# Kernel optimization log

Hardware: AMD Instinct MI355X
Metric: run time of the kernel (lower is better)

## Reference

```python
import jax, jax.numpy as jnp
import numpy as np

WIN = (8, 8)
NUM_HEADS = 8
DIM = 256


def _relative_position_index(wh, ww):
    ch = np.arange(wh)
    cw = np.arange(ww)
    coords = np.stack(np.meshgrid(ch, cw, indexing='ij'))  # [2, wh, ww]
    cf = coords.reshape(2, -1)                              # [2, N]
    rel = cf[:, :, None] - cf[:, None, :]                   # [2, N, N]
    rel = rel.transpose(1, 2, 0).copy()
    rel[:, :, 0] += wh - 1
    rel[:, :, 1] += ww - 1
    rel[:, :, 0] *= 2 * ww - 1
    return rel.sum(-1).astype(np.int32)                     # [N, N]


def setup_inputs() -> dict:
    key = jax.random.key(0)
    ks = jax.random.split(key, 7)
    N = WIN[0] * WIN[1]
    BW = 4096  # num_windows * batch
    x = jax.random.normal(ks[0], (BW, N, DIM), dtype=jnp.float32)
    # 0 / -inf style shift mask; random 0 or -100 per entry for generality
    mask = jnp.where(jax.random.uniform(ks[1], (BW, N, N)) < 0.2, -100.0, 0.0).astype(jnp.float32)
    rpb_table = jax.random.normal(ks[2], ((2 * WIN[0] - 1) * (2 * WIN[1] - 1), NUM_HEADS), dtype=jnp.float32) * 0.02
    qkv_w = jax.random.normal(ks[3], (3 * DIM, DIM), dtype=jnp.float32) * (DIM ** -0.5)
    qkv_b = jax.random.normal(ks[4], (3 * DIM,), dtype=jnp.float32) * 0.01
    proj_w = jax.random.normal(ks[5], (DIM, DIM), dtype=jnp.float32) * (DIM ** -0.5)
    proj_b = jax.random.normal(ks[6], (DIM,), dtype=jnp.float32) * 0.01
    rel_idx = jnp.asarray(_relative_position_index(*WIN))
    return {"x": x, "mask": mask, "rpb_table": rpb_table, "qkv_w": qkv_w,
            "qkv_b": qkv_b, "proj_w": proj_w, "proj_b": proj_b, "rel_idx": rel_idx}


def reference(x, mask, rpb_table, qkv_w, qkv_b, proj_w, proj_b, rel_idx):
    B_, N, C = x.shape
    H = NUM_HEADS
    hd = C // H
    scale = hd ** -0.5
    qkv = x @ qkv_w.T + qkv_b                               # [B_, N, 3C]
    qkv = qkv.reshape(B_, N, 3, H, hd).transpose(2, 0, 3, 1, 4)  # [3, B_, H, N, hd]
    q, k, v = qkv[0], qkv[1], qkv[2]
    attn = jnp.einsum('bhnd,bhmd->bhnm', q * scale, k)      # [B_, H, N, N]
    bias = rpb_table[rel_idx.reshape(-1)].reshape(N, N, H).transpose(2, 0, 1)  # [H, N, N]
    attn = attn + bias[None]
    nW = mask.shape[0]
    attn = attn.reshape(B_ // nW, nW, H, N, N) + mask[None, :, None]
    attn = attn.reshape(B_, H, N, N)
    attn = jax.nn.softmax(attn, axis=-1)
    out = jnp.einsum('bhnm,bhmd->bhnd', attn, v)            # [B_, H, N, hd]
    out = out.transpose(0, 2, 1, 3).reshape(B_, N, C)
    return out @ proj_w.T + proj_b
```

## Files before the change

### kernel.cpp

```cpp
#include <hip/hip_runtime.h>

typedef _Float16 half_t;
typedef __attribute__((ext_vector_type(8))) _Float16 half8;
typedef __attribute__((ext_vector_type(4))) float f32x4;

#define WS_W1   0
#define WS_W2   (768*256*2)
#define WS_BIAS (WS_W2 + 256*256*2)
#define QK_SCALE 0.17677669529663687f

__global__ __launch_bounds__(256) void prep_kernel(
    const float* __restrict__ qkv_w, const float* __restrict__ proj_w,
    const float* __restrict__ rpb, const int* __restrict__ rel_idx,
    char* __restrict__ ws) {
  int tid = blockIdx.x * 256 + threadIdx.x;
  half_t* W1 = (half_t*)(ws + WS_W1);
  half_t* W2 = (half_t*)(ws + WS_W2);
  float* BIASP = (float*)(ws + WS_BIAS);
  if (tid < 768 * 256) {
    int n = tid >> 8;
    float v = qkv_w[tid];
    if (n < 256) v *= QK_SCALE;
    W1[tid] = (half_t)v;
  }
  if (tid < 256 * 256) W2[tid] = (half_t)proj_w[tid];
  if (tid < 8 * 4096) {
    int r   = tid & 3;
    int l16 = (tid >> 2) & 15;
    int q   = (tid >> 6) & 3;
    int nt  = (tid >> 8) & 3;
    int mt  = (tid >> 10) & 3;
    int h   = (tid >> 12) & 7;
    int i = 16 * mt + 4 * q + r;
    int j = 16 * nt + l16;
    BIASP[tid] = rpb[rel_idx[i * 64 + j] * 8 + h];
  }
}

__global__ __launch_bounds__(512, 2) void fused_kernel(
    const float* __restrict__ x, const float* __restrict__ mask,
    const float* __restrict__ qkv_b, const float* __restrict__ proj_b,
    const char* __restrict__ ws, float* __restrict__ out, int nW) {
  __shared__ __align__(16) half_t Xs[64 * 264];
  __shared__ __align__(16) half_t QK[8][2][64 * 40];
  __shared__ __align__(16) half_t VT[8][32 * 72];
  __shared__ __align__(16) half_t Ms[64 * 68];

  const int b = blockIdx.x;
  const int tid = threadIdx.x;
  const int wave = tid >> 6, lane = tid & 63;
  const int l16 = lane & 15, quad = lane >> 4;
  const f32x4 z4 = {0.f, 0.f, 0.f, 0.f};

  {
    const float4* xw = (const float4*)(x + (size_t)b * 16384);
#pragma unroll
    for (int i = 0; i < 8; ++i) {
      int idx4 = tid + i * 512;
      float4 v = xw[idx4];
      int e = idx4 << 2;
      int row = e >> 8, col = e & 255;
      union { half_t h[4]; long long ll; } pk;
      pk.h[0] = (half_t)v.x; pk.h[1] = (half_t)v.y;
      pk.h[2] = (half_t)v.z; pk.h[3] = (half_t)v.w;
      *(long long*)(&Xs[row * 264 + col]) = pk.ll;
    }
    const float4* mw = (const float4*)(mask + (size_t)(b % nW) * 4096);
#pragma unroll
    for (int i = 0; i < 2; ++i) {
      int idx4 = tid + i * 512;
      float4 v = mw[idx4];
      int e = idx4 << 2;
      int mi = e >> 6, mj = e & 63;
      union { half_t h[4]; long long ll; } pk;
      pk.h[0] = (half_t)v.x; pk.h[1] = (half_t)v.y;
      pk.h[2] = (half_t)v.z; pk.h[3] = (half_t)v.w;
      *(long long*)(&Ms[mi * 68 + mj]) = pk.ll;
    }
  }
  __syncthreads();

  {
    const half_t* W1 = (const half_t*)(ws + WS_W1);
    const int nwb = wave * 96;
    f32x4 acc[6][4];
#pragma unroll
    for (int nt = 0; nt < 6; ++nt)
#pragma unroll
      for (int mt = 0; mt < 4; ++mt) acc[nt][mt] = z4;
#pragma unroll
    for (int ks = 0; ks < 8; ++ks) {
      half8 af[4];
#pragma unroll
      for (int mt = 0; mt < 4; ++mt)
        af[mt] = *(const half8*)(&Xs[(16 * mt + l16) * 264 + 32 * ks + quad * 8]);
#pragma unroll
      for (int nt = 0; nt < 6; ++nt) {
        half8 bf = *(const half8*)(&W1[(size_t)(nwb + 16 * nt + l16) * 256 + 32 * ks + quad * 8]);
#pragma unroll
        for (int mt = 0; mt < 4; ++mt)
          acc[nt][mt] = __builtin_amdgcn_mfma_f32_16x16x32_f16(af[mt], bf, acc[nt][mt], 0, 0, 0);
      }
    }
#pragma unroll
    for (int nt = 0; nt < 6; ++nt) {
      int n = nwb + 16 * nt + l16;
      float bias = qkv_b[n];
      int part = n >> 8;
      if (part == 0) bias *= QK_SCALE;
      int h = (n >> 5) & 7;
      int d = n & 31;
#pragma unroll
      for (int mt = 0; mt < 4; ++mt) {
#pragma unroll
        for (int r = 0; r < 4; ++r) {
          int t = 16 * mt + quad * 4 + r;
          float v = acc[nt][mt][r] + bias;
          if (part < 2) QK[h][part][t * 40 + d] = (half_t)v;
          else          VT[h][d * 72 + t] = (half_t)v;
        }
      }
    }
  }
  __syncthreads();

  {
    const int h = wave;
    const half_t* Qh = &QK[h][0][0];
    const half_t* Kh = &QK[h][1][0];
    const half_t* Vh = &VT[h][0];
    half8 qf[4], kf[4];
#pragma unroll
    for (int mt = 0; mt < 4; ++mt)
      qf[mt] = *(const half8*)(Qh + (16 * mt + l16) * 40 + quad * 8);
#pragma unroll
    for (int nt = 0; nt < 4; ++nt)
      kf[nt] = *(const half8*)(Kh + (16 * nt + l16) * 40 + quad * 8);
    f32x4 S[4][4];
#pragma unroll
    for (int mt = 0; mt < 4; ++mt)
#pragma unroll
      for (int nt = 0; nt < 4; ++nt)
        S[mt][nt] = __builtin_amdgcn_mfma_f32_16x16x32_f16(qf[mt], kf[nt], z4, 0, 0, 0);

    const float4* BP4 = (const float4*)(ws + WS_BIAS);
    float linv[4][4];
#pragma unroll
    for (int mt = 0; mt < 4; ++mt) {
#pragma unroll
      for (int nt = 0; nt < 4; ++nt) {
        float4 bv = BP4[(size_t)(((h * 4 + mt) * 4 + nt) * 64) + quad * 16 + l16];
#pragma unroll
        for (int r = 0; r < 4; ++r)
          S[mt][nt][r] += ((const float*)&bv)[r] +
                          (float)Ms[(16 * mt + quad * 4 + r) * 68 + 16 * nt + l16];
      }
#pragma unroll
      for (int r = 0; r < 4; ++r) {
        float mx = fmaxf(fmaxf(S[mt][0][r], S[mt][1][r]), fmaxf(S[mt][2][r], S[mt][3][r]));
#pragma unroll
        for (int o = 1; o < 16; o <<= 1) mx = fmaxf(mx, __shfl_xor(mx, o, 64));
        float s = 0.f;
#pragma unroll
        for (int nt = 0; nt < 4; ++nt) {
          float e = exp2f((S[mt][nt][r] - mx) * 1.44269504f);
          S[mt][nt][r] = e;
          s += e;
        }
#pragma unroll
        for (int o = 1; o < 16; o <<= 1) s += __shfl_xor(s, o, 64);
        linv[mt][r] = 1.f / s;
      }
    }

    half8 vf[2][2];
#pragma unroll
    for (int nt = 0; nt < 2; ++nt)
#pragma unroll
      for (int ks = 0; ks < 2; ++ks)
        vf[nt][ks] = *(const half8*)(Vh + (16 * nt + l16) * 72 + 32 * ks + quad * 8);
    half_t* P = &QK[h][0][0];
#pragma unroll
    for (int mt = 0; mt < 4; ++mt) {
#pragma unroll
      for (int nt = 0; nt < 4; ++nt)
#pragma unroll
        for (int r = 0; r < 4; ++r)
          P[(quad * 4 + r) * 72 + 16 * nt + l16] = (half_t)(S[mt][nt][r] * linv[mt][r]);
      f32x4 O[2] = {z4, z4};
#pragma unroll
      for (int ks = 0; ks < 2; ++ks) {
        half8 pf = *(const half8*)(P + l16 * 72 + 32 * ks + quad * 8);
#pragma unroll
        for (int nt = 0; nt < 2; ++nt)
          O[nt] = __builtin_amdgcn_mfma_f32_16x16x32_f16(pf, vf[nt][ks], O[nt], 0, 0, 0);
      }
#pragma unroll
      for (int nt = 0; nt < 2; ++nt)
#pragma unroll
        for (int r = 0; r < 4; ++r)
          Xs[(16 * mt + quad * 4 + r) * 264 + h * 32 + 16 * nt + l16] = (half_t)O[nt][r];
    }
  }
  __syncthreads();

  {
    const half_t* W2 = (const half_t*)(ws + WS_W2);
    const int nb = wave * 32;
    f32x4 C[2][4];
#pragma unroll
    for (int nt = 0; nt < 2; ++nt)
#pragma unroll
      for (int mt = 0; mt < 4; ++mt) C[nt][mt] = z4;
#pragma unroll
    for (int ks = 0; ks < 8; ++ks) {
      half8 af[4];
#pragma unroll
      for (int mt = 0; mt < 4; ++mt)
        af[mt] = *(const half8*)(&Xs[(16 * mt + l16) * 264 + 32 * ks + quad * 8]);
#pragma unroll
      for (int nt = 0; nt < 2; ++nt) {
        half8 bf = *(const half8*)(&W2[(size_t)(nb + 16 * nt + l16) * 256 + 32 * ks + quad * 8]);
#pragma unroll
        for (int mt = 0; mt < 4; ++mt)
          C[nt][mt] = __builtin_amdgcn_mfma_f32_16x16x32_f16(af[mt], bf, C[nt][mt], 0, 0, 0);
      }
    }
#pragma unroll
    for (int nt = 0; nt < 2; ++nt) {
      int c = nb + 16 * nt + l16;
      float pb = proj_b[c];
#pragma unroll
      for (int mt = 0; mt < 4; ++mt)
#pragma unroll
        for (int r = 0; r < 4; ++r) {
          int t = 16 * mt + quad * 4 + r;
          out[(size_t)b * 16384 + t * 256 + c] = C[nt][mt][r] + pb;
        }
    }
  }
}

extern "C" void kernel_launch(void* const* d_in, const int* in_sizes, int n_in,
                              void* d_out, int out_size, void* d_ws, size_t ws_size,
                              hipStream_t stream) {
  const float* x      = (const float*)d_in[0];
  const float* mask   = (const float*)d_in[1];
  const float* rpb    = (const float*)d_in[2];
  const float* qkv_w  = (const float*)d_in[3];
  const float* qkv_b  = (const float*)d_in[4];
  const float* proj_w = (const float*)d_in[5];
  const float* proj_b = (const float*)d_in[6];
  const int*   rel    = (const int*)d_in[7];
  float* out = (float*)d_out;
  char* ws = (char*)d_ws;
  int B_ = in_sizes[0] / 16384;
  int nW = in_sizes[1] / 4096;
  hipLaunchKernelGGL(prep_kernel, dim3(768), dim3(256), 0, stream,
                     qkv_w, proj_w, rpb, rel, ws);
  hipLaunchKernelGGL(fused_kernel, dim3(B_), dim3(512), 0, stream,
                     x, mask, qkv_b, proj_b, (const char*)ws, out, nW);
}
```

Baseline: 845.8 us.

## Compute per-head QKV inside each wave to shrink LDS and raise occupancy

Each wave now computes only its own head's V, Q and K projections in sequence and stages them through a small per-wave scratch buffer. This replaces the shared QK/VT buffers and removes one block-wide barrier. The smaller LDS footprint and register use allow launch bounds of 4 blocks per CU instead of 2. Softmax normalization is deferred to the output via a fast reciprocal, and an extra barrier protects Xs before the attention output is written back. Occupancy may be limited by register pressure, since the O accumulators stay live across all of attention.

```diff
diff --git a/kernel.cpp b/kernel.cpp
--- a/kernel.cpp
+++ b/kernel.cpp
@@ -1,6 +1,7 @@
 #include <hip/hip_runtime.h>
 
 typedef _Float16 half_t;
+typedef __attribute__((ext_vector_type(4))) _Float16 half4;
 typedef __attribute__((ext_vector_type(8))) _Float16 half8;
 typedef __attribute__((ext_vector_type(4))) float f32x4;
 
@@ -37,20 +38,40 @@
   }
 }
 
-__global__ __launch_bounds__(512, 2) void fused_kernel(
+__device__ __forceinline__ void qkv_gemm(const half_t* Xs, const half_t* W1,
+                                         int n0, int l16, int quad,
+                                         f32x4 acc[2][4]) {
+#pragma unroll
+  for (int ks = 0; ks < 8; ++ks) {
+    half8 af[4];
+#pragma unroll
+    for (int mt = 0; mt < 4; ++mt)
+      af[mt] = *(const half8*)(&Xs[(16 * mt + l16) * 264 + 32 * ks + quad * 8]);
+#pragma unroll
+    for (int nt = 0; nt < 2; ++nt) {
+      half8 bf = *(const half8*)(&W1[(size_t)(n0 + 16 * nt + l16) * 256 + 32 * ks + quad * 8]);
+#pragma unroll
+      for (int mt = 0; mt < 4; ++mt)
+        acc[nt][mt] = __builtin_amdgcn_mfma_f32_16x16x32_f16(af[mt], bf, acc[nt][mt], 0, 0, 0);
+    }
+  }
+}
+
+__global__ __launch_bounds__(512, 4) void fused_kernel(
     const float* __restrict__ x, const float* __restrict__ mask,
     const float* __restrict__ qkv_b, const float* __restrict__ proj_b,
     const char* __restrict__ ws, float* __restrict__ out, int nW) {
   __shared__ __align__(16) half_t Xs[64 * 264];
-  __shared__ __align__(16) half_t QK[8][2][64 * 40];
-  __shared__ __align__(16) half_t VT[8][32 * 72];
   __shared__ __align__(16) half_t Ms[64 * 68];
+  __shared__ __align__(16) half_t Scr[8][2304];
 
   const int b = blockIdx.x;
   const int tid = threadIdx.x;
   const int wave = tid >> 6, lane = tid & 63;
   const int l16 = lane & 15, quad = lane >> 4;
   const f32x4 z4 = {0.f, 0.f, 0.f, 0.f};
+  const half_t* W1 = (const half_t*)(ws + WS_W1);
+  half_t* Sw = &Scr[wave][0];
 
   {
     const float4* xw = (const float4*)(x + (size_t)b * 16384);
@@ -60,10 +81,9 @@
       float4 v = xw[idx4];
       int e = idx4 << 2;
       int row = e >> 8, col = e & 255;
-      union { half_t h[4]; long long ll; } pk;
-      pk.h[0] = (half_t)v.x; pk.h[1] = (half_t)v.y;
-      pk.h[2] = (half_t)v.z; pk.h[3] = (half_t)v.w;
-      *(long long*)(&Xs[row * 264 + col]) = pk.ll;
+      half4 pk;
+      pk[0] = (half_t)v.x; pk[1] = (half_t)v.y; pk[2] = (half_t)v.z; pk[3] = (half_t)v.w;
+      *(half4*)(&Xs[row * 264 + col]) = pk;
     }
     const float4* mw = (const float4*)(mask + (size_t)(b % nW) * 4096);
 #pragma unroll
@@ -72,79 +92,114 @@
       float4 v = mw[idx4];
       int e = idx4 << 2;
       int mi = e >> 6, mj = e & 63;
-      union { half_t h[4]; long long ll; } pk;
-      pk.h[0] = (half_t)v.x; pk.h[1] = (half_t)v.y;
-      pk.h[2] = (half_t)v.z; pk.h[3] = (half_t)v.w;
-      *(long long*)(&Ms[mi * 68 + mj]) = pk.ll;
+      half4 pk;
+      pk[0] = (half_t)v.x; pk[1] = (half_t)v.y; pk[2] = (half_t)v.z; pk[3] = (half_t)v.w;
+      *(half4*)(&Ms[mi * 68 + mj]) = pk;
     }
   }
   __syncthreads();
 
-  {
-    const half_t* W1 = (const half_t*)(ws + WS_W1);
-    const int nwb = wave * 96;
-    f32x4 acc[6][4];
-#pragma unroll
-    for (int nt = 0; nt < 6; ++nt)
+  const int h = wave;
+  half8 vf[2][2];
+  half8 qf[4];
+  f32x4 S[4][4];
+  f32x4 O[4][2];
+  float linv[4][4];
+
+  {
+    f32x4 acc[2][4];
+#pragma unroll
+    for (int nt = 0; nt < 2; ++nt)
 #pragma unroll
       for (int mt = 0; mt < 4; ++mt) acc[nt][mt] = z4;
-#pragma unroll
-    for (int ks = 0; ks < 8; ++ks) {
-      half8 af[4];
-#pragma unroll
-      for (int mt = 0; mt < 4; ++mt)
-        af[mt] = *(const half8*)(&Xs[(16 * mt + l16) * 264 + 32 * ks + quad * 8]);
-#pragma unroll
-      for (int nt = 0; nt < 6; ++nt) {
-        half8 bf = *(const half8*)(&W1[(size_t)(nwb + 16 * nt + l16) * 256 + 32 * ks + quad * 8]);
-#pragma unroll
-        for (int mt = 0; mt < 4; ++mt)
-          acc[nt][mt] = __builtin_amdgcn_mfma_f32_16x16x32_f16(af[mt], bf, acc[nt][mt], 0, 0, 0);
-      }
-    }
-#pragma unroll
-    for (int nt = 0; nt < 6; ++nt) {
-      int n = nwb + 16 * nt + l16;
-      float bias = qkv_b[n];
-      int part = n >> 8;
-      if (part == 0) bias *= QK_SCALE;
-      int h = (n >> 5) & 7;
-      int d = n & 31;
+    const int n0 = 512 + 32 * h;
+    qkv_gemm(Xs, W1, n0, l16, quad, acc);
+#pragma unroll
+    for (int nt = 0; nt < 2; ++nt) {
+      float vb = qkv_b[n0 + 16 * nt + l16];
 #pragma unroll
       for (int mt = 0; mt < 4; ++mt) {
-#pragma unroll
-        for (int r = 0; r < 4; ++r) {
-          int t = 16 * mt + quad * 4 + r;
-          float v = acc[nt][mt][r] + bias;
-          if (part < 2) QK[h][part][t * 40 + d] = (half_t)v;
-          else          VT[h][d * 72 + t] = (half_t)v;
-        }
-      }
-    }
-  }
-  __syncthreads();
-
-  {
-    const int h = wave;
-    const half_t* Qh = &QK[h][0][0];
-    const half_t* Kh = &QK[h][1][0];
-    const half_t* Vh = &VT[h][0];
-    half8 qf[4], kf[4];
-#pragma unroll
-    for (int mt = 0; mt < 4; ++mt)
-      qf[mt] = *(const half8*)(Qh + (16 * mt + l16) * 40 + quad * 8);
-#pragma unroll
-    for (int nt = 0; nt < 4; ++nt)
-      kf[nt] = *(const half8*)(Kh + (16 * nt + l16) * 40 + quad * 8);
-    f32x4 S[4][4];
-#pragma unroll
-    for (int mt = 0; mt < 4; ++mt)
-#pragma unroll
-      for (int nt = 0; nt < 4; ++nt)
-        S[mt][nt] = __builtin_amdgcn_mfma_f32_16x16x32_f16(qf[mt], kf[nt], z4, 0, 0, 0);
-
+        half4 pk;
+#pragma unroll
+        for (int r = 0; r < 4; ++r) pk[r] = (half_t)(acc[nt][mt][r] + vb);
+        *(half4*)(&Sw[(16 * nt + l16) * 72 + 16 * mt + 4 * quad]) = pk;
+      }
+    }
+#pragma unroll
+    for (int nt = 0; nt < 2; ++nt)
+#pragma unroll
+      for (int ks = 0; ks < 2; ++ks)
+        vf[nt][ks] = *(const half8*)(&Sw[(16 * nt + l16) * 72 + 32 * ks + quad * 8]);
+    asm volatile("s_waitcnt lgkmcnt(0)" ::: "memory");
+  }
+
+  {
+    f32x4 acc[2][4];
+#pragma unroll
+    for (int nt = 0; nt < 2; ++nt)
+#pragma unroll
+      for (int mt = 0; mt < 4; ++mt) acc[nt][mt] = z4;
+    const int n0 = 32 * h;
+    qkv_gemm(Xs, W1, n0, l16, quad, acc);
+#pragma unroll
+    for (int nt = 0; nt < 2; ++nt) {
+      float qb = qkv_b[n0 + 16 * nt + l16] * QK_SCALE;
+#pragma unroll
+      for (int mt = 0; mt < 4; ++mt)
+#pragma unroll
+        for (int r = 0; r < 4; ++r)
+          Sw[(16 * mt + 4 * quad + r) * 36 + 16 * nt + l16] = (half_t)(acc[nt][mt][r] + qb);
+    }
+#pragma unroll
+    for (int mt = 0; mt < 4; ++mt) {
+      union { half8 v; half4 hh[2]; } u;
+      u.hh[0] = *(const half4*)(&Sw[(16 * mt + l16) * 36 + quad * 8]);
+      u.hh[1] = *(const half4*)(&Sw[(16 * mt + l16) * 36 + quad * 8 + 4]);
+      qf[mt] = u.v;
+    }
+    asm volatile("s_waitcnt lgkmcnt(0)" ::: "memory");
+  }
+
+  {
+    f32x4 acc[2][4];
+#pragma unroll
+    for (int nt = 0; nt < 2; ++nt)
+#pragma unroll
+      for (int mt = 0; mt < 4; ++mt) acc[nt][mt] = z4;
+    const int n0 = 256 + 32 * h;
+    qkv_gemm(Xs, W1, n0, l16, quad, acc);
+#pragma unroll
+    for (int nt = 0; nt < 2; ++nt) {
+      float kb = qkv_b[n0 + 16 * nt + l16];
+#pragma unroll
+      for (int mt = 0; mt < 4; ++mt)
+#pragma unroll
+        for (int r = 0; r < 4; ++r)
+          Sw[(16 * mt + 4 * quad + r) * 36 + 16 * nt + l16] = (half_t)(acc[nt][mt][r] + kb);
+    }
+#pragma unroll
+    for (int kh = 0; kh < 2; ++kh) {
+      half8 kf[2];
+#pragma unroll
+      for (int n2 = 0; n2 < 2; ++n2) {
+        int jt = 2 * kh + n2;
+        union { half8 v; half4 hh[2]; } u;
+        u.hh[0] = *(const half4*)(&Sw[(16 * jt + l16) * 36 + quad * 8]);
+        u.hh[1] = *(const half4*)(&Sw[(16 * jt + l16) * 36 + quad * 8 + 4]);
+        kf[n2] = u.v;
+      }
+#pragma unroll
+      for (int mt = 0; mt < 4; ++mt)
+#pragma unroll
+        for (int n2 = 0; n2 < 2; ++n2)
+          S[mt][2 * kh + n2] =
+              __builtin_amdgcn_mfma_f32_16x16x32_f16(qf[mt], kf[n2], z4, 0, 0, 0);
+    }
+    asm volatile("s_waitcnt lgkmcnt(0)" ::: "memory");
+  }
+
+  {
     const float4* BP4 = (const float4*)(ws + WS_BIAS);
-    float linv[4][4];
 #pragma unroll
     for (int mt = 0; mt < 4; ++mt) {
 #pragma unroll
@@ -153,7 +208,7 @@
 #pragma unroll
         for (int r = 0; r < 4; ++r)
           S[mt][nt][r] += ((const float*)&bv)[r] +
-                          (float)Ms[(16 * mt + quad * 4 + r) * 68 + 16 * nt + l16];
+                          (float)Ms[(16 * mt + 4 * quad + r) * 68 + 16 * nt + l16];
       }
 #pragma unroll
       for (int r = 0; r < 4; ++r) {
@@ -169,39 +224,37 @@
         }
 #pragma unroll
         for (int o = 1; o < 16; o <<= 1) s += __shfl_xor(s, o, 64);
-        linv[mt][r] = 1.f / s;
-      }
-    }
-
-    half8 vf[2][2];
-#pragma unroll
-    for (int nt = 0; nt < 2; ++nt)
-#pragma unroll
-      for (int ks = 0; ks < 2; ++ks)
-        vf[nt][ks] = *(const half8*)(Vh + (16 * nt + l16) * 72 + 32 * ks + quad * 8);
-    half_t* P = &QK[h][0][0];
-#pragma unroll
-    for (int mt = 0; mt < 4; ++mt) {
+        linv[mt][r] = __builtin_amdgcn_rcpf(s);
+      }
 #pragma unroll
       for (int nt = 0; nt < 4; ++nt)
 #pragma unroll
         for (int r = 0; r < 4; ++r)
-          P[(quad * 4 + r) * 72 + 16 * nt + l16] = (half_t)(S[mt][nt][r] * linv[mt][r]);
-      f32x4 O[2] = {z4, z4};
+          Sw[(4 * quad + r) * 72 + 16 * nt + l16] = (half_t)S[mt][nt][r];
+      f32x4 o0 = z4, o1 = z4;
 #pragma unroll
       for (int ks = 0; ks < 2; ++ks) {
-        half8 pf = *(const half8*)(P + l16 * 72 + 32 * ks + quad * 8);
-#pragma unroll
-        for (int nt = 0; nt < 2; ++nt)
-          O[nt] = __builtin_amdgcn_mfma_f32_16x16x32_f16(pf, vf[nt][ks], O[nt], 0, 0, 0);
-      }
-#pragma unroll
-      for (int nt = 0; nt < 2; ++nt)
-#pragma unroll
-        for (int r = 0; r < 4; ++r)
-          Xs[(16 * mt + quad * 4 + r) * 264 + h * 32 + 16 * nt + l16] = (half_t)O[nt][r];
-    }
-  }
+        half8 pf = *(const half8*)(&Sw[l16 * 72 + 32 * ks + quad * 8]);
+        o0 = __builtin_amdgcn_mfma_f32_16x16x32_f16(pf, vf[0][ks], o0, 0, 0, 0);
+        o1 = __builtin_amdgcn_mfma_f32_16x16x32_f16(pf, vf[1][ks], o1, 0, 0, 0);
+      }
+#pragma unroll
+      for (int r = 0; r < 4; ++r) {
+        O[mt][0][r] = o0[r] * linv[mt][r];
+        O[mt][1][r] = o1[r] * linv[mt][r];
+      }
+      asm volatile("s_waitcnt lgkmcnt(0)" ::: "memory");
+    }
+  }
+  __syncthreads();
+
+#pragma unroll
+  for (int mt = 0; mt < 4; ++mt)
+#pragma unroll
+    for (int nt = 0; nt < 2; ++nt)
+#pragma unroll
+      for (int r = 0; r < 4; ++r)
+        Xs[(16 * mt + 4 * quad + r) * 264 + 32 * h + 16 * nt + l16] = (half_t)O[mt][nt][r];
   __syncthreads();
 
   {
@@ -234,7 +287,7 @@
       for (int mt = 0; mt < 4; ++mt)
 #pragma unroll
         for (int r = 0; r < 4; ++r) {
-          int t = 16 * mt + quad * 4 + r;
+          int t = 16 * mt + 4 * quad + r;
           out[(size_t)b * 16384 + t * 256 + c] = C[nt][mt][r] + pb;
         }
     }
```

Result: faster. 816.8 us (-3.4%).
